# Performance work log

Hardware: AMD Instinct MI355X
Metric: run time of the kernel (lower is better)

The kernel has to match this reference:

```python
import jax, jax.numpy as jnp
import numpy as np

B, L, C_S, H = 1, 512, 384, 12
D = C_S // H  # head_dim = 32


def setup_inputs() -> dict:
    key = jax.random.key(0)
    ks = jax.random.split(key, 12)
    sc = 1.0 / np.sqrt(C_S)
    inp = {
        "s": jax.random.normal(ks[0], (B, L, C_S), dtype=jnp.float32),
        "z": jax.random.normal(ks[1], (B, L, L, C_S), dtype=jnp.float32),
        "mask": jax.random.randint(ks[2], (B, L), 0, 2, dtype=jnp.int32),
        # learned params
        "Wq": jax.random.normal(ks[3], (C_S, H * D), dtype=jnp.float32) * sc,
        "bq": jnp.zeros((H * D,), dtype=jnp.float32),
        "Wkv": jax.random.normal(ks[4], (C_S, 2 * H * D), dtype=jnp.float32) * sc,
        "bkv": jnp.zeros((2 * H * D,), dtype=jnp.float32),
        "Wb": jax.random.normal(ks[5], (C_S, H), dtype=jnp.float32) * sc,
        "bb": jnp.zeros((H,), dtype=jnp.float32),
        "Wg": jax.random.normal(ks[6], (C_S, H), dtype=jnp.float32) * sc,
        "bg": jnp.zeros((H,), dtype=jnp.float32),
        "Wout": jax.random.normal(ks[7], (H * D, C_S), dtype=jnp.float32) * sc,
        "bout": jnp.zeros((C_S,), dtype=jnp.float32),
    }
    return inp


def reference(s, z, Wq, bq, Wkv, bkv, Wb, bb, Wg, bg, Wout, bout, mask):
    b, l, c = s.shape
    q = (s @ Wq + bq).reshape(b, l, H, D)                 # (B,L,h,d)
    kv = (s @ Wkv + bkv).reshape(b, l, 2, H, D)
    k, v = kv[:, :, 0], kv[:, :, 1]                       # (B,L,h,d)
    logits = jnp.einsum('blhd,bmhd->bhlm', q, k) * (D ** -0.5)
    bias = jnp.transpose(z @ Wb + bb, (0, 3, 1, 2))       # (B,h,L,L)
    logits = logits + bias
    gate = jax.nn.sigmoid(jnp.transpose(z @ Wg + bg, (0, 3, 1, 2)))
    maskf = mask.astype(logits.dtype)
    mask2d = maskf[:, :, None] * maskf[:, None, :]        # (B,L,L)
    logits = jnp.where(mask2d[:, None] < 0.5, jnp.asarray(-1e9, logits.dtype), logits)
    attn = jax.nn.softmax(logits, axis=-1) * gate         # (B,h,L,L)
    o = jnp.einsum('bhlm,bmhd->blhd', attn, v).reshape(b, l, H * D)
    return o @ Wout + bout
```

## Files before the change

### kernel.cpp

```cpp
#include <hip/hip_runtime.h>
#include <math.h>


typedef float vf4 __attribute__((ext_vector_type(4)));
typedef __attribute__((address_space(3))) void       lds_vp;
typedef __attribute__((address_space(1))) const void gm_vp;

__global__ __launch_bounds__(256) void sgemm_bias(const float* __restrict__ A, int lda,
                                                  const float* __restrict__ B, int ldb,
                                                  const float* __restrict__ bias,
                                                  float* __restrict__ C, int ldc, int K)
{
    __shared__ float As[32 * 36];
    __shared__ float Bs[32 * 68];

    const int t  = threadIdx.x;
    const int m0 = blockIdx.y * 32;
    const int n0 = blockIdx.x * 64;
    const int tx = t & 15;
    const int ty = t >> 4;

    float acc[2][4];
    #pragma unroll
    for (int i = 0; i < 2; ++i)
        #pragma unroll
        for (int j = 0; j < 4; ++j) acc[i][j] = 0.f;

    for (int kc = 0; kc < K; kc += 32) {
        __syncthreads();
        {
            int r = t >> 3, c = (t & 7) * 4;
            float4 av = *(const float4*)&A[(size_t)(m0 + r) * lda + kc + c];
            As[(c + 0) * 36 + r] = av.x;
            As[(c + 1) * 36 + r] = av.y;
            As[(c + 2) * 36 + r] = av.z;
            As[(c + 3) * 36 + r] = av.w;
        }
        #pragma unroll
        for (int i = 0; i < 2; ++i) {
            int slot = i * 256 + t;
            int r = slot >> 4, c = (slot & 15) * 4;
            *(float4*)&Bs[r * 68 + c] = *(const float4*)&B[(size_t)(kc + r) * ldb + n0 + c];
        }
        __syncthreads();
        #pragma unroll 8
        for (int k = 0; k < 32; ++k) {
            float2 a = *(const float2*)&As[k * 36 + ty * 2];
            float4 b = *(const float4*)&Bs[k * 68 + tx * 4];
            acc[0][0] = fmaf(a.x, b.x, acc[0][0]);
            acc[0][1] = fmaf(a.x, b.y, acc[0][1]);
            acc[0][2] = fmaf(a.x, b.z, acc[0][2]);
            acc[0][3] = fmaf(a.x, b.w, acc[0][3]);
            acc[1][0] = fmaf(a.y, b.x, acc[1][0]);
            acc[1][1] = fmaf(a.y, b.y, acc[1][1]);
            acc[1][2] = fmaf(a.y, b.z, acc[1][2]);
            acc[1][3] = fmaf(a.y, b.w, acc[1][3]);
        }
    }

    float4 bv = *(const float4*)&bias[n0 + tx * 4];
    #pragma unroll
    for (int im = 0; im < 2; ++im) {
        float4 r;
        r.x = acc[im][0] + bv.x;
        r.y = acc[im][1] + bv.y;
        r.z = acc[im][2] + bv.z;
        r.w = acc[im][3] + bv.w;
        *(float4*)&C[(size_t)(m0 + ty * 2 + im) * ldc + n0 + tx * 4] = r;
    }
}

__global__ __launch_bounds__(256) void wcat_kernel(const float* __restrict__ Wb,
                                                   const float* __restrict__ Wg,
                                                   float* __restrict__ wcat)
{
    int idx = blockIdx.x * 256 + threadIdx.x;
    if (idx < 24 * 384) {
        int hh = idx / 384, k = idx % 384;
        wcat[idx] = (hh < 12) ? Wb[k * 12 + hh] : Wg[k * 12 + (hh - 12)];
    }
}

__global__ __launch_bounds__(256) void biasgate_kernel(const float* __restrict__ z,
                                                       const float* __restrict__ wcat,
                                                       const float* __restrict__ bb,
                                                       const float* __restrict__ bg,
                                                       float* __restrict__ bias_out,
                                                       float* __restrict__ gate_out)
{
    __shared__ float zt[2][256 * 32];

    const int t  = threadIdx.x;
    const size_t p0 = (size_t)blockIdx.x * 256;
    const size_t p  = p0 + t;

    const int wv   = t >> 6;
    const int lane = t & 63;
    const int lrow = lane >> 3;
    const int lcol = (lane & 7) * 4;

    float acc[24];
    #pragma unroll
    for (int h = 0; h < 24; ++h) acc[h] = 0.f;

    #pragma unroll
    for (int i = 0; i < 8; ++i) {
        const int row = wv * 64 + i * 8 + lrow;
        __builtin_amdgcn_global_load_lds(
            (gm_vp*)(z + (p0 + row) * 384 + lcol),
            (lds_vp*)(&zt[0][row * 32 + lcol]), 16, 0, 0);
    }
    __syncthreads();

    #pragma unroll 1
    for (int c = 0; c < 12; ++c) {
        const int cur = c & 1;
        if (c < 11) {
            const int nk = (c + 1) * 32;
            #pragma unroll
            for (int i = 0; i < 8; ++i) {
                const int row = wv * 64 + i * 8 + lrow;
                __builtin_amdgcn_global_load_lds(
                    (gm_vp*)(z + (p0 + row) * 384 + nk + lcol),
                    (lds_vp*)(&zt[cur ^ 1][row * 32 + lcol]), 16, 0, 0);
            }
        }
        const int kc = c * 32;
        #pragma unroll
        for (int k4 = 0; k4 < 8; ++k4) {
            const vf4 zv = *(const vf4*)&zt[cur][t * 32 + k4 * 4];
            const float* wp = wcat + kc + k4 * 4;
            #pragma unroll
            for (int hh = 0; hh < 24; ++hh) {
                float4 w = *(const float4*)&wp[hh * 384];
                acc[hh] = fmaf(zv.x, w.x,
                          fmaf(zv.y, w.y,
                          fmaf(zv.z, w.z,
                          fmaf(zv.w, w.w, acc[hh]))));
            }
        }
        __syncthreads();
    }

    #pragma unroll
    for (int hh = 0; hh < 12; ++hh)
        bias_out[(size_t)hh * 262144 + p] = acc[hh] + bb[hh];
    #pragma unroll
    for (int hh = 0; hh < 12; ++hh) {
        float x = acc[12 + hh] + bg[hh];
        gate_out[(size_t)hh * 262144 + p] = 1.f / (1.f + expf(-x));
    }
}

__global__ __launch_bounds__(256) void attn_kernel(const float* __restrict__ q_ws,
                                                   const float* __restrict__ kv_ws,
                                                   const float* __restrict__ bias_ws,
                                                   const float* __restrict__ gate_ws,
                                                   const int* __restrict__ mask,
                                                   float* __restrict__ o_ws)
{
    __shared__ float ql[16 * 36];
    __shared__ float kl[128 * 36];
    __shared__ float att[16 * 516];
    __shared__ int   mint[16];

    const int t  = threadIdx.x;
    const int h  = blockIdx.y;
    const int i0 = blockIdx.x * 16;

    for (int idx = t; idx < 512; idx += 256) {
        int ii = idx >> 5, d = idx & 31;
        ql[ii * 36 + d] = q_ws[(size_t)(i0 + ii) * 384 + h * 32 + d];
    }
    if (t < 16) mint[t] = mask[i0 + t];

    const float inv = 0.17677669529663687f;
    const int jl = t & 127;
    const int ip = t >> 7;

    for (int jc = 0; jc < 4; ++jc) {
        const int j0 = jc * 128;
        __syncthreads();
        for (int idx = t; idx < 4096; idx += 256) {
            int jj = idx >> 5, d = idx & 31;
            kl[jj * 36 + d] = kv_ws[(size_t)(j0 + jj) * 768 + h * 32 + d];
        }
        __syncthreads();
        float4 kr[8];
        #pragma unroll
        for (int x = 0; x < 8; ++x) kr[x] = *(const float4*)&kl[jl * 36 + x * 4];
        const int mj = mask[j0 + jl];
        #pragma unroll
        for (int rr = 0; rr < 8; ++rr) {
            int ii = ip + rr * 2;
            float dot = 0.f;
            #pragma unroll
            for (int x = 0; x < 8; ++x) {
                float4 qv = *(const float4*)&ql[ii * 36 + x * 4];
                dot = fmaf(kr[x].x, qv.x, dot);
                dot = fmaf(kr[x].y, qv.y, dot);
                dot = fmaf(kr[x].z, qv.z, dot);
                dot = fmaf(kr[x].w, qv.w, dot);
            }
            float bv = bias_ws[((size_t)h << 18) + (size_t)(i0 + ii) * 512 + j0 + jl];
            float lg = fmaf(dot, inv, bv);
            att[ii * 516 + j0 + jl] = (mint[ii] != 0 && mj != 0) ? lg : -1e9f;
        }
    }
    __syncthreads();

    {
        const int rr = t >> 4, g = t & 15;
        const int base = rr * 516 + g;
        float mx = -3.0e38f;
        #pragma unroll
        for (int n = 0; n < 32; ++n) mx = fmaxf(mx, att[base + n * 16]);
        #pragma unroll
        for (int off = 8; off >= 1; off >>= 1) mx = fmaxf(mx, __shfl_xor(mx, off));
        float sum = 0.f;
        #pragma unroll
        for (int n = 0; n < 32; ++n) {
            float e = expf(att[base + n * 16] - mx);
            att[base + n * 16] = e;
            sum += e;
        }
        #pragma unroll
        for (int off = 8; off >= 1; off >>= 1) sum += __shfl_xor(sum, off);
        float isum = 1.f / sum;
        const size_t gbase = ((size_t)h << 18) + (size_t)(i0 + rr) * 512 + g;
        #pragma unroll
        for (int n = 0; n < 32; ++n) {
            float gt = gate_ws[gbase + n * 16];
            att[base + n * 16] *= isum * gt;
        }
    }
    __syncthreads();

    {
        const int d = t & 31, grp = t >> 5;
        const float* vp = kv_ws + 384 + h * 32 + d;
        float a0 = 0.f, a1 = 0.f;
        #pragma unroll 8
        for (int j = 0; j < 512; ++j) {
            float vv = vp[(size_t)j * 768];
            a0 = fmaf(att[grp * 516 + j], vv, a0);
            a1 = fmaf(att[(grp + 8) * 516 + j], vv, a1);
        }
        o_ws[(size_t)(i0 + grp) * 384 + h * 32 + d]     = a0;
        o_ws[(size_t)(i0 + grp + 8) * 384 + h * 32 + d] = a1;
    }
}

extern "C" void kernel_launch(void* const* d_in, const int* in_sizes, int n_in,
                              void* d_out, int out_size, void* d_ws, size_t ws_size,
                              hipStream_t stream)
{
    const float* s    = (const float*)d_in[0];
    const float* z    = (const float*)d_in[1];
    const int*   mask = (const int*)  d_in[2];
    const float* Wq   = (const float*)d_in[3];
    const float* bq   = (const float*)d_in[4];
    const float* Wkv  = (const float*)d_in[5];
    const float* bkv  = (const float*)d_in[6];
    const float* Wb   = (const float*)d_in[7];
    const float* bb   = (const float*)d_in[8];
    const float* Wg   = (const float*)d_in[9];
    const float* bg   = (const float*)d_in[10];
    const float* Wout = (const float*)d_in[11];
    const float* bout = (const float*)d_in[12];
    float* out = (float*)d_out;

    float* ws      = (float*)d_ws;
    float* q_ws    = ws;
    float* kv_ws   = q_ws + 512 * 384;
    float* o_ws    = kv_ws + 512 * 768;
    float* bias_ws = o_ws + 512 * 384;
    float* gate_ws = bias_ws + 12 * 512 * 512;
    float* wcat_ws = gate_ws + 12 * 512 * 512;

    wcat_kernel<<<36, 256, 0, stream>>>(Wb, Wg, wcat_ws);
    sgemm_bias<<<dim3(384 / 64, 512 / 32), 256, 0, stream>>>(s, 384, Wq, 384, bq, q_ws, 384, 384);
    sgemm_bias<<<dim3(768 / 64, 512 / 32), 256, 0, stream>>>(s, 384, Wkv, 768, bkv, kv_ws, 768, 384);
    biasgate_kernel<<<1024, 256, 0, stream>>>(z, wcat_ws, bb, bg, bias_ws, gate_ws);
    attn_kernel<<<dim3(512 / 16, 12), 256, 0, stream>>>(q_ws, kv_ws, bias_ws, gate_ws, mask, o_ws);
    sgemm_bias<<<dim3(384 / 64, 512 / 32), 256, 0, stream>>>(o_ws, 384, Wout, 384, bout, out, 384, 384);
}
```

Baseline: 766.4 us.

## Make bias/gate projection stage per-wavefront with swizzled LDS and vmcnt waits

Rewrites the z-projection kernel so each wavefront loads and consumes only its own 64 rows of z. This replaces the block-wide __syncthreads with s_waitcnt vmcnt waits on the async global-to-LDS loads. It adds an XOR swizzle on LDS columns to avoid bank conflicts when each thread reads its own row. Double buffering is kept per wave with two chunks in flight. The risk is correctness if the vmcnt counting does not match the number of outstanding loads. The last iteration also redundantly reloads a chunk.

```diff
diff --git a/kernel.cpp b/kernel.cpp
--- a/kernel.cpp
+++ b/kernel.cpp
@@ -88,68 +88,82 @@
                                                        float* __restrict__ bias_out,
                                                        float* __restrict__ gate_out)
 {
-    __shared__ float zt[2][256 * 32];
-
-    const int t  = threadIdx.x;
+    __shared__ float bufA[4][64 * 32];
+    __shared__ float bufB[4][64 * 32];
+
+    const int t     = threadIdx.x;
     const size_t p0 = (size_t)blockIdx.x * 256;
-    const size_t p  = p0 + t;
-
-    const int wv   = t >> 6;
-    const int lane = t & 63;
-    const int lrow = lane >> 3;
-    const int lcol = (lane & 7) * 4;
+    const int wv    = t >> 6;
+    const int lane  = t & 63;
+    const int lrow  = lane >> 3;
+    const int lcol  = (lane & 7) * 4;
+    const int scol  = lcol ^ (lrow << 2);
+
+    const float* zsrc = z + (p0 + (size_t)(wv * 64 + lrow)) * 384 + scol;
+    float* ldsA = &bufA[wv][0];
+    float* ldsB = &bufB[wv][0];
+    const int r  = lane;
+    const int r7 = t & 7;
 
     float acc[24];
     #pragma unroll
     for (int h = 0; h < 24; ++h) acc[h] = 0.f;
 
-    #pragma unroll
-    for (int i = 0; i < 8; ++i) {
-        const int row = wv * 64 + i * 8 + lrow;
-        __builtin_amdgcn_global_load_lds(
-            (gm_vp*)(z + (p0 + row) * 384 + lcol),
-            (lds_vp*)(&zt[0][row * 32 + lcol]), 16, 0, 0);
-    }
-    __syncthreads();
+#define BG_STAGE(LDS, C)                                                    \
+    {                                                                       \
+        const int kc_ = (C) * 32;                                           \
+        _Pragma("unroll")                                                   \
+        for (int i = 0; i < 8; ++i)                                         \
+            __builtin_amdgcn_global_load_lds(                               \
+                (gm_vp*)(zsrc + (size_t)i * 3072 + kc_),                    \
+                (lds_vp*)((LDS) + i * 256), 16, 0, 0);                      \
+    }
+
+#define BG_COMPUTE(LDS, C)                                                  \
+    {                                                                       \
+        const int kc_ = (C) * 32;                                           \
+        _Pragma("unroll")                                                   \
+        for (int k4 = 0; k4 < 8; ++k4) {                                    \
+            const vf4 zv = *(const vf4*)((LDS) + r * 32 + ((k4 ^ r7) << 2)); \
+            const float* wp = wcat + kc_ + k4 * 4;                          \
+            _Pragma("unroll")                                               \
+            for (int hh = 0; hh < 24; ++hh) {                               \
+                float4 w = *(const float4*)&wp[hh * 384];                   \
+                acc[hh] = fmaf(zv.x, w.x, fmaf(zv.y, w.y,                   \
+                          fmaf(zv.z, w.z, fmaf(zv.w, w.w, acc[hh]))));      \
+            }                                                               \
+        }                                                                   \
+    }
+
+#define BG_WAIT8 asm volatile("s_waitcnt vmcnt(8)" ::: "memory")
+#define BG_WAIT0 asm volatile("s_waitcnt vmcnt(0)" ::: "memory")
+
+    BG_STAGE(ldsA, 0);
+    BG_STAGE(ldsB, 1);
 
     #pragma unroll 1
-    for (int c = 0; c < 12; ++c) {
-        const int cur = c & 1;
-        if (c < 11) {
-            const int nk = (c + 1) * 32;
-            #pragma unroll
-            for (int i = 0; i < 8; ++i) {
-                const int row = wv * 64 + i * 8 + lrow;
-                __builtin_amdgcn_global_load_lds(
-                    (gm_vp*)(z + (p0 + row) * 384 + nk + lcol),
-                    (lds_vp*)(&zt[cur ^ 1][row * 32 + lcol]), 16, 0, 0);
-            }
-        }
-        const int kc = c * 32;
-        #pragma unroll
-        for (int k4 = 0; k4 < 8; ++k4) {
-            const vf4 zv = *(const vf4*)&zt[cur][t * 32 + k4 * 4];
-            const float* wp = wcat + kc + k4 * 4;
-            #pragma unroll
-            for (int hh = 0; hh < 24; ++hh) {
-                float4 w = *(const float4*)&wp[hh * 384];
-                acc[hh] = fmaf(zv.x, w.x,
-                          fmaf(zv.y, w.y,
-                          fmaf(zv.z, w.z,
-                          fmaf(zv.w, w.w, acc[hh]))));
-            }
-        }
-        __syncthreads();
-    }
+    for (int c = 0; c < 12; c += 2) {
+        BG_WAIT8;
+        BG_COMPUTE(ldsA, c);
+        BG_STAGE(ldsA, (c + 2 < 12) ? c + 2 : c);
+        BG_WAIT8;
+        BG_COMPUTE(ldsB, c + 1);
+        if (c + 3 < 12) BG_STAGE(ldsB, c + 3);
+    }
+    BG_WAIT0;
 
     #pragma unroll
     for (int hh = 0; hh < 12; ++hh)
-        bias_out[(size_t)hh * 262144 + p] = acc[hh] + bb[hh];
+        bias_out[(size_t)hh * 262144 + p0 + t] = acc[hh] + bb[hh];
     #pragma unroll
     for (int hh = 0; hh < 12; ++hh) {
         float x = acc[12 + hh] + bg[hh];
-        gate_out[(size_t)hh * 262144 + p] = 1.f / (1.f + expf(-x));
-    }
+        gate_out[(size_t)hh * 262144 + p0 + t] = 1.f / (1.f + expf(-x));
+    }
+#undef BG_STAGE
+#undef BG_COMPUTE
+#undef BG_WAIT8
+#undef BG_WAIT0
 }
 
 __global__ __launch_bounds__(256) void attn_kernel(const float* __restrict__ q_ws,
```

Result: slower. 974.9 us (+27.2%).
